# Kernel optimization log

Hardware: AMD Instinct MI355X
Metric: run time of the kernel (lower is better)

## Reference

```python
import jax, jax.numpy as jnp
import numpy as np

# Grid parameters (from init_kwargs)
GRID_W, GRID_L, GRID_H = 96, 96, 48
VOXEL_SIZE = 0.05
MIN_POINTS_PER_VOXEL = 10


def setup_inputs() -> dict:
    key = jax.random.key(0)
    k1, k2 = jax.random.split(key, 2)
    # points uniform over a ~[0,1.5]^3 sub-volume so voxel occupancy is realistic
    point_coordinates = jax.random.uniform(k1, (4, 3, 480, 640), jnp.float32) * 1.5
    point_attributes = jax.random.normal(k2, (4, 16, 480, 640), jnp.float32)
    origin = jnp.zeros((4, 3), jnp.float32)
    return {"point_coordinates": point_coordinates,
            "point_attributes": point_attributes,
            "origin": origin}


def _voxelize_one(coords, attrs, org):
    # coords: [3, N], attrs: [C, N], org: [3]
    V = GRID_W * GRID_L * GRID_H
    bounds = jnp.array([GRID_W, GRID_L, GRID_H], jnp.int32)
    # per-point voxel index (floor == .long() for positive; OOB handled by mask)
    idx3 = jnp.floor((coords - org[:, None]) / VOXEL_SIZE).astype(jnp.int32)  # [3, N]
    in_bounds = jnp.all((idx3 >= 0) & (idx3 < bounds[:, None]), axis=0)       # [N]
    flat = idx3[0] * (GRID_L * GRID_H) + idx3[1] * GRID_H + idx3[2]           # [N]
    flat = jnp.where(in_bounds, flat, 0)  # route OOB points to voxel 0, masked out
    # occupancy: scatter-add of in-bounds mask
    counts = jax.ops.segment_sum(in_bounds.astype(jnp.float32), flat, num_segments=V)
    # max-pool of attributes per voxel; OOB points contribute -inf
    masked = jnp.where(in_bounds[None, :], attrs, -jnp.inf)                   # [C, N]
    vmax = jax.ops.segment_max(masked.T, flat, num_segments=V).T              # [C, V]
    occ = counts >= MIN_POINTS_PER_VOXEL                                      # [V]
    data = jnp.where(occ[None, :] & jnp.isfinite(vmax), vmax, 0.0)            # [C, V]
    return data, occ


def reference(point_coordinates, point_attributes, origin):
    b, c = point_attributes.shape[:2]
    coords = point_coordinates.reshape(b, 3, -1)   # [B, 3, N]
    attrs = point_attributes.reshape(b, c, -1)     # [B, C, N]
    data, occ = jax.vmap(_voxelize_one)(coords, attrs, origin)
    voxeldata = data.reshape(b, c, GRID_W, GRID_L, GRID_H)
    voxeloccupancy = occ.reshape(b, 1, GRID_W, GRID_L, GRID_H).astype(jnp.float32)
    return voxeldata, voxeloccupancy
```

## Files before the change

### kernel.cpp

```cpp
#include <hip/hip_runtime.h>
#include <cstdint>
#include <math.h>

#define GRID_W 96
#define GRID_L 96
#define GRID_H 48
#define NVOX (GRID_W * GRID_L * GRID_H)
#define VOXEL_SIZE 0.05f
#define MIN_PTS 10
#define BATCH 4
#define CHANS 16
#define NPTS (480 * 640)
#define TOTPTS (BATCH * NPTS)
#define TOTVOX (BATCH * NVOX)

#define SCAN_BLKS 864
#define SCAN_TPB 256
#define SCAN_EPT 8
#define SCAN_CHUNK (SCAN_TPB * SCAN_EPT)

#define WS_OFFSETS 0
#define WS_VR      ((TOTVOX + 4) * 4)
#define WS_ROWS    (WS_VR + TOTPTS * 4)
#define WS_SUMS    (WS_ROWS + (size_t)TOTPTS * CHANS * 4)
#define WS_NEEDED  ((size_t)(WS_SUMS + 4096))


__global__ void k_zero(uint4* __restrict__ off4, unsigned* __restrict__ offsets) {
    int i = blockIdx.x * blockDim.x + threadIdx.x;
    if (i < TOTVOX / 4) off4[i] = uint4{0u, 0u, 0u, 0u};
    if (i == 0) {
        offsets[TOTVOX + 0] = 0u; offsets[TOTVOX + 1] = 0u;
        offsets[TOTVOX + 2] = 0u; offsets[TOTVOX + 3] = 0u;
    }
}

__global__ void k_hist4(const float* __restrict__ coords,
                        const float* __restrict__ origin,
                        unsigned*    __restrict__ vr,
                        unsigned*    __restrict__ cnt)
{
    int t = blockIdx.x * blockDim.x + threadIdx.x;
    if (t >= TOTPTS / 4) return;
    int pid = t * 4;
    int b = pid / NPTS;
    int n = pid - b * NPTS;

    const float* cb = coords + (size_t)b * 3 * NPTS;
    float4 X = *(const float4*)(cb + n);
    float4 Y = *(const float4*)(cb + NPTS + n);
    float4 Z = *(const float4*)(cb + 2 * NPTS + n);
    float ox = origin[b * 3 + 0];
    float oy = origin[b * 3 + 1];
    float oz = origin[b * 3 + 2];

    float xs[4] = {X.x, X.y, X.z, X.w};
    float ys[4] = {Y.x, Y.y, Y.z, Y.w};
    float zs[4] = {Z.x, Z.y, Z.z, Z.w};
    unsigned ps[4];
    #pragma unroll
    for (int k = 0; k < 4; ++k) {
        int ix = (int)floorf((xs[k] - ox) / VOXEL_SIZE);
        int iy = (int)floorf((ys[k] - oy) / VOXEL_SIZE);
        int iz = (int)floorf((zs[k] - oz) / VOXEL_SIZE);
        unsigned p = 0xFFFFFFFFu;
        if ((unsigned)ix < GRID_W && (unsigned)iy < GRID_L && (unsigned)iz < GRID_H) {
            int v = b * NVOX + ix * (GRID_L * GRID_H) + iy * GRID_H + iz;
            unsigned r = atomicAdd(&cnt[v], 1u);
            p = ((unsigned)v << 10) | (r & 1023u);
        }
        ps[k] = p;
    }
    *(uint4*)(vr + pid) = uint4{ps[0], ps[1], ps[2], ps[3]};
}

__global__ void k_scan1(unsigned* __restrict__ offsets,
                        unsigned* __restrict__ sums,
                        float*    __restrict__ occ)
{
    __shared__ unsigned s[SCAN_TPB];
    int t = threadIdx.x;
    int base = blockIdx.x * SCAN_CHUNK + t * SCAN_EPT;

    uint4 a = ((const uint4*)(offsets + base))[0];
    uint4 c = ((const uint4*)(offsets + base))[1];
    unsigned e[SCAN_EPT] = {a.x, a.y, a.z, a.w, c.x, c.y, c.z, c.w};

    float4 oc0, oc1;
    oc0.x = (e[0] >= MIN_PTS) ? 1.f : 0.f;  oc0.y = (e[1] >= MIN_PTS) ? 1.f : 0.f;
    oc0.z = (e[2] >= MIN_PTS) ? 1.f : 0.f;  oc0.w = (e[3] >= MIN_PTS) ? 1.f : 0.f;
    oc1.x = (e[4] >= MIN_PTS) ? 1.f : 0.f;  oc1.y = (e[5] >= MIN_PTS) ? 1.f : 0.f;
    oc1.z = (e[6] >= MIN_PTS) ? 1.f : 0.f;  oc1.w = (e[7] >= MIN_PTS) ? 1.f : 0.f;
    ((float4*)(occ + base))[0] = oc0;
    ((float4*)(occ + base))[1] = oc1;

    unsigned tot = 0;
    #pragma unroll
    for (int k = 0; k < SCAN_EPT; ++k) { unsigned v = e[k]; e[k] = tot; tot += v; }

    s[t] = tot;
    __syncthreads();
    #pragma unroll
    for (int off = 1; off < SCAN_TPB; off <<= 1) {
        unsigned v = (t >= off) ? s[t - off] : 0u;
        __syncthreads();
        s[t] += v;
        __syncthreads();
    }
    unsigned prefix = s[t] - tot;
    #pragma unroll
    for (int k = 0; k < SCAN_EPT; ++k) e[k] += prefix;

    ((uint4*)(offsets + base))[0] = uint4{e[0], e[1], e[2], e[3]};
    ((uint4*)(offsets + base))[1] = uint4{e[4], e[5], e[6], e[7]};

    if (t == SCAN_TPB - 1) sums[blockIdx.x] = s[t];
}

__global__ void k_scan2(unsigned* __restrict__ sums) {
    __shared__ unsigned s[1024];
    int t = threadIdx.x;
    unsigned my = (t < SCAN_BLKS) ? sums[t] : 0u;
    s[t] = my;
    __syncthreads();
    #pragma unroll
    for (int off = 1; off < 1024; off <<= 1) {
        unsigned v = (t >= off) ? s[t - off] : 0u;
        __syncthreads();
        s[t] += v;
        __syncthreads();
    }
    if (t < SCAN_BLKS) sums[t] = s[t] - my;
    if (t == SCAN_BLKS - 1) sums[SCAN_BLKS] = s[t];
}

__global__ void k_scatter_rows(const float*    __restrict__ attrs,
                               const unsigned* __restrict__ vr,
                               const unsigned* __restrict__ offsets,
                               const unsigned* __restrict__ sums,
                               float*          __restrict__ rows)
{
    int id = blockIdx.x * blockDim.x + threadIdx.x;
    if (id >= TOTPTS) return;
    unsigned p = vr[id];
    if (p == 0xFFFFFFFFu) return;
    unsigned v = p >> 10;
    unsigned r = p & 1023u;
    unsigned pos = offsets[v] + sums[v >> 11] + r;

    int b = id / NPTS;
    int n = id - b * NPTS;
    const float* ab = attrs + (size_t)b * CHANS * NPTS + n;
    float4 r0, r1, r2, r3;
    r0.x = ab[0 * (size_t)NPTS];  r0.y = ab[1 * (size_t)NPTS];
    r0.z = ab[2 * (size_t)NPTS];  r0.w = ab[3 * (size_t)NPTS];
    r1.x = ab[4 * (size_t)NPTS];  r1.y = ab[5 * (size_t)NPTS];
    r1.z = ab[6 * (size_t)NPTS];  r1.w = ab[7 * (size_t)NPTS];
    r2.x = ab[8 * (size_t)NPTS];  r2.y = ab[9 * (size_t)NPTS];
    r2.z = ab[10 * (size_t)NPTS]; r2.w = ab[11 * (size_t)NPTS];
    r3.x = ab[12 * (size_t)NPTS]; r3.y = ab[13 * (size_t)NPTS];
    r3.z = ab[14 * (size_t)NPTS]; r3.w = ab[15 * (size_t)NPTS];

    float4* dst = (float4*)(rows + (size_t)pos * CHANS);
    dst[0] = r0; dst[1] = r1; dst[2] = r2; dst[3] = r3;
}

__global__ void k_gather_rows(const float*    __restrict__ rows,
                              const unsigned* __restrict__ offsets,
                              const unsigned* __restrict__ sums,
                              float*          __restrict__ data)
{
    int vox = blockIdx.x * blockDim.x + threadIdx.x;
    if (vox >= TOTVOX) return;

    unsigned s0 = offsets[vox] + sums[vox >> 11];
    unsigned s1 = offsets[vox + 1] + sums[(vox + 1) >> 11];
    unsigned k = s1 - s0;

    float4 m0 = {0.f,0.f,0.f,0.f}, m1 = m0, m2 = m0, m3 = m0;
    if (k >= MIN_PTS) {
        const float ninf = -__builtin_inff();
        m0 = m1 = m2 = m3 = float4{ninf, ninf, ninf, ninf};
        const float4* seg = (const float4*)(rows + (size_t)s0 * CHANS);
        for (unsigned j = 0; j < k; ++j) {
            float4 r0 = seg[0], r1 = seg[1], r2 = seg[2], r3 = seg[3];
            seg += 4;
            m0.x = fmaxf(m0.x, r0.x); m0.y = fmaxf(m0.y, r0.y);
            m0.z = fmaxf(m0.z, r0.z); m0.w = fmaxf(m0.w, r0.w);
            m1.x = fmaxf(m1.x, r1.x); m1.y = fmaxf(m1.y, r1.y);
            m1.z = fmaxf(m1.z, r1.z); m1.w = fmaxf(m1.w, r1.w);
            m2.x = fmaxf(m2.x, r2.x); m2.y = fmaxf(m2.y, r2.y);
            m2.z = fmaxf(m2.z, r2.z); m2.w = fmaxf(m2.w, r2.w);
            m3.x = fmaxf(m3.x, r3.x); m3.y = fmaxf(m3.y, r3.y);
            m3.z = fmaxf(m3.z, r3.z); m3.w = fmaxf(m3.w, r3.w);
        }
        float mv[16] = {m0.x,m0.y,m0.z,m0.w, m1.x,m1.y,m1.z,m1.w,
                        m2.x,m2.y,m2.z,m2.w, m3.x,m3.y,m3.z,m3.w};
        #pragma unroll
        for (int c = 0; c < CHANS; ++c) if (!isfinite(mv[c])) mv[c] = 0.f;
        m0 = float4{mv[0],mv[1],mv[2],mv[3]};   m1 = float4{mv[4],mv[5],mv[6],mv[7]};
        m2 = float4{mv[8],mv[9],mv[10],mv[11]}; m3 = float4{mv[12],mv[13],mv[14],mv[15]};
    }

    int b = vox / NVOX;
    int v = vox - b * NVOX;
    float* db = data + (size_t)b * CHANS * NVOX + v;
    db[0 * (size_t)NVOX] = m0.x;  db[1 * (size_t)NVOX] = m0.y;
    db[2 * (size_t)NVOX] = m0.z;  db[3 * (size_t)NVOX] = m0.w;
    db[4 * (size_t)NVOX] = m1.x;  db[5 * (size_t)NVOX] = m1.y;
    db[6 * (size_t)NVOX] = m1.z;  db[7 * (size_t)NVOX] = m1.w;
    db[8 * (size_t)NVOX] = m2.x;  db[9 * (size_t)NVOX] = m2.y;
    db[10 * (size_t)NVOX] = m2.z; db[11 * (size_t)NVOX] = m2.w;
    db[12 * (size_t)NVOX] = m3.x; db[13 * (size_t)NVOX] = m3.y;
    db[14 * (size_t)NVOX] = m3.z; db[15 * (size_t)NVOX] = m3.w;
}


__device__ __forceinline__ unsigned flip_f32(float f) {
    unsigned u = __float_as_uint(f);
    unsigned mask = (unsigned)(-(int)(u >> 31)) | 0x80000000u;
    return u ^ mask;
}
__device__ __forceinline__ float unflip_f32(unsigned u) {
    unsigned mask = ((u >> 31) - 1u) | 0x80000000u;
    return __uint_as_float(u ^ mask);
}
#define FLIP_NEG_INF 0x007FFFFFu

__global__ void pv_init(uint4* __restrict__ out) {
    const int DATA4 = BATCH * CHANS * NVOX / 4;
    const int TOT4  = BATCH * (CHANS + 1) * NVOX / 4;
    int i = blockIdx.x * blockDim.x + threadIdx.x;
    if (i < TOT4) {
        unsigned val = (i < DATA4) ? FLIP_NEG_INF : 0u;
        out[i] = uint4{val, val, val, val};
    }
}

__global__ void pv_scatter(const float* __restrict__ coords,
                           const float* __restrict__ attrs,
                           const float* __restrict__ origin,
                           unsigned*    __restrict__ data_u,
                           unsigned*    __restrict__ cnt)
{
    int id = blockIdx.x * blockDim.x + threadIdx.x;
    if (id >= TOTPTS) return;
    int b = id / NPTS;
    int n = id - b * NPTS;
    const float* cb = coords + (size_t)b * 3 * NPTS;
    float x = cb[n], y = cb[NPTS + n], z = cb[2 * NPTS + n];
    float ox = origin[b * 3 + 0], oy = origin[b * 3 + 1], oz = origin[b * 3 + 2];
    int ix = (int)floorf((x - ox) / VOXEL_SIZE);
    int iy = (int)floorf((y - oy) / VOXEL_SIZE);
    int iz = (int)floorf((z - oz) / VOXEL_SIZE);
    if ((unsigned)ix < GRID_W && (unsigned)iy < GRID_L && (unsigned)iz < GRID_H) {
        int flat = ix * (GRID_L * GRID_H) + iy * GRID_H + iz;
        atomicAdd(&cnt[b * NVOX + flat], 1u);
        const float* ab = attrs + (size_t)b * CHANS * NPTS + n;
        unsigned*    db = data_u + (size_t)b * CHANS * NVOX + flat;
        #pragma unroll
        for (int c = 0; c < CHANS; ++c)
            atomicMax(&db[(size_t)c * NVOX], flip_f32(ab[(size_t)c * NPTS]));
    }
}

__global__ void pv_finalize(unsigned* __restrict__ data_u,
                            unsigned* __restrict__ cnt_u)
{
    int id = blockIdx.x * blockDim.x + threadIdx.x;
    if (id >= TOTVOX) return;
    int b = id / NVOX;
    int v = id - b * NVOX;
    unsigned cnt = cnt_u[id];
    bool occ = (cnt >= MIN_PTS);
    ((float*)cnt_u)[id] = occ ? 1.0f : 0.0f;
    unsigned* db = data_u + (size_t)b * CHANS * NVOX + v;
    #pragma unroll
    for (int c = 0; c < CHANS; ++c) {
        float f = unflip_f32(db[(size_t)c * NVOX]);
        ((float*)db)[(size_t)c * NVOX] = (occ && isfinite(f)) ? f : 0.0f;
    }
}


extern "C" void kernel_launch(void* const* d_in, const int* in_sizes, int n_in,
                              void* d_out, int out_size, void* d_ws, size_t ws_size,
                              hipStream_t stream) {
    const float* coords = (const float*)d_in[0];
    const float* attrs  = (const float*)d_in[1];
    const float* origin = (const float*)d_in[2];

    float* out = (float*)d_out;
    float* data = out;
    float* occ  = out + (size_t)BATCH * CHANS * NVOX;

    if (ws_size >= WS_NEEDED) {
        char* ws = (char*)d_ws;
        unsigned* offsets = (unsigned*)(ws + WS_OFFSETS);
        unsigned* vr      = (unsigned*)(ws + WS_VR);
        float*    rows    = (float*)(ws + WS_ROWS);
        unsigned* sums    = (unsigned*)(ws + WS_SUMS);

        k_zero<<<(TOTVOX / 4 + 255) / 256, 256, 0, stream>>>((uint4*)offsets, offsets);
        k_hist4<<<(TOTPTS / 4 + 255) / 256, 256, 0, stream>>>(coords, origin, vr, offsets);
        k_scan1<<<SCAN_BLKS, SCAN_TPB, 0, stream>>>(offsets, sums, occ);
        k_scan2<<<1, 1024, 0, stream>>>(sums);
        k_scatter_rows<<<(TOTPTS + 255) / 256, 256, 0, stream>>>(attrs, vr, offsets, sums, rows);
        k_gather_rows<<<(TOTVOX + 255) / 256, 256, 0, stream>>>(rows, offsets, sums, data);
    } else {
        unsigned* data_u = (unsigned*)data;
        unsigned* cnt    = (unsigned*)occ;
        const int TOT4 = BATCH * (CHANS + 1) * NVOX / 4;
        pv_init<<<(TOT4 + 255) / 256, 256, 0, stream>>>((uint4*)d_out);
        pv_scatter<<<(TOTPTS + 255) / 256, 256, 0, stream>>>(coords, attrs, origin, data_u, cnt);
        pv_finalize<<<(TOTVOX + 255) / 256, 256, 0, stream>>>(data_u, cnt);
    }
}
```

Baseline: 343.2 us.

## Pack intermediate rows as bf16 and vectorize scatter/gather four-wide

The permuted per-point attribute rows in the workspace are now stored as bf16 pairs (8 words per point instead of 16 floats), which halves the scatter write and gather read traffic. The scatter and gather kernels now handle four points or four voxels per thread, using float4/uint4 loads and stores. The zeroing kernel is replaced by hipMemsetAsync. The bf16 rounding changes the max-pooled output values, so results lose precision relative to the fp32 reference and may fail tolerance checks.

```diff
diff --git a/kernel.cpp b/kernel.cpp
--- a/kernel.cpp
+++ b/kernel.cpp
@@ -19,21 +19,22 @@
 #define SCAN_EPT 8
 #define SCAN_CHUNK (SCAN_TPB * SCAN_EPT)
 
+#define ROWW 8
+
 #define WS_OFFSETS 0
 #define WS_VR      ((TOTVOX + 4) * 4)
 #define WS_ROWS    (WS_VR + TOTPTS * 4)
-#define WS_SUMS    (WS_ROWS + (size_t)TOTPTS * CHANS * 4)
+#define WS_SUMS    (WS_ROWS + (size_t)TOTPTS * ROWW * 4)
 #define WS_NEEDED  ((size_t)(WS_SUMS + 4096))
 
-
-__global__ void k_zero(uint4* __restrict__ off4, unsigned* __restrict__ offsets) {
-    int i = blockIdx.x * blockDim.x + threadIdx.x;
-    if (i < TOTVOX / 4) off4[i] = uint4{0u, 0u, 0u, 0u};
-    if (i == 0) {
-        offsets[TOTVOX + 0] = 0u; offsets[TOTVOX + 1] = 0u;
-        offsets[TOTVOX + 2] = 0u; offsets[TOTVOX + 3] = 0u;
-    }
-}
+__device__ __forceinline__ unsigned bf16_rtne(float f) {
+    unsigned u = __float_as_uint(f);
+    return (u + 0x7FFFu + ((u >> 16) & 1u)) >> 16;
+}
+__device__ __forceinline__ unsigned pack2(float lo, float hi) {
+    return bf16_rtne(lo) | (bf16_rtne(hi) << 16);
+}
+
 
 __global__ void k_hist4(const float* __restrict__ coords,
                         const float* __restrict__ origin,
@@ -134,85 +135,101 @@
     if (t == SCAN_BLKS - 1) sums[SCAN_BLKS] = s[t];
 }
 
-__global__ void k_scatter_rows(const float*    __restrict__ attrs,
-                               const unsigned* __restrict__ vr,
+__global__ void k_scatter_rows4(const float*    __restrict__ attrs,
+                                const unsigned* __restrict__ vr,
+                                const unsigned* __restrict__ offsets,
+                                const unsigned* __restrict__ sums,
+                                unsigned*       __restrict__ rows)
+{
+    int t = blockIdx.x * blockDim.x + threadIdx.x;
+    if (t >= TOTPTS / 4) return;
+    int pid = t * 4;
+    int b = pid / NPTS;
+    int n = pid - b * NPTS;
+
+    uint4 P = *(const uint4*)(vr + pid);
+    unsigned ps[4] = {P.x, P.y, P.z, P.w};
+    unsigned pos[4];
+    #pragma unroll
+    for (int k = 0; k < 4; ++k) {
+        pos[k] = 0xFFFFFFFFu;
+        if (ps[k] != 0xFFFFFFFFu) {
+            unsigned v = ps[k] >> 10;
+            pos[k] = offsets[v] + sums[v >> 11] + (ps[k] & 1023u);
+        }
+    }
+
+    const float* ab = attrs + (size_t)b * CHANS * NPTS + n;
+    unsigned w[4][ROWW];
+    #pragma unroll
+    for (int c = 0; c < CHANS; c += 2) {
+        float4 a0 = *(const float4*)(ab + (size_t)c * NPTS);
+        float4 a1 = *(const float4*)(ab + (size_t)(c + 1) * NPTS);
+        w[0][c >> 1] = pack2(a0.x, a1.x);
+        w[1][c >> 1] = pack2(a0.y, a1.y);
+        w[2][c >> 1] = pack2(a0.z, a1.z);
+        w[3][c >> 1] = pack2(a0.w, a1.w);
+    }
+    #pragma unroll
+    for (int k = 0; k < 4; ++k) {
+        if (pos[k] == 0xFFFFFFFFu) continue;
+        uint4* dst = (uint4*)(rows + (size_t)pos[k] * ROWW);
+        dst[0] = uint4{w[k][0], w[k][1], w[k][2], w[k][3]};
+        dst[1] = uint4{w[k][4], w[k][5], w[k][6], w[k][7]};
+    }
+}
+
+__global__ void k_gather_rows4(const unsigned* __restrict__ rows,
                                const unsigned* __restrict__ offsets,
                                const unsigned* __restrict__ sums,
-                               float*          __restrict__ rows)
-{
-    int id = blockIdx.x * blockDim.x + threadIdx.x;
-    if (id >= TOTPTS) return;
-    unsigned p = vr[id];
-    if (p == 0xFFFFFFFFu) return;
-    unsigned v = p >> 10;
-    unsigned r = p & 1023u;
-    unsigned pos = offsets[v] + sums[v >> 11] + r;
-
-    int b = id / NPTS;
-    int n = id - b * NPTS;
-    const float* ab = attrs + (size_t)b * CHANS * NPTS + n;
-    float4 r0, r1, r2, r3;
-    r0.x = ab[0 * (size_t)NPTS];  r0.y = ab[1 * (size_t)NPTS];
-    r0.z = ab[2 * (size_t)NPTS];  r0.w = ab[3 * (size_t)NPTS];
-    r1.x = ab[4 * (size_t)NPTS];  r1.y = ab[5 * (size_t)NPTS];
-    r1.z = ab[6 * (size_t)NPTS];  r1.w = ab[7 * (size_t)NPTS];
-    r2.x = ab[8 * (size_t)NPTS];  r2.y = ab[9 * (size_t)NPTS];
-    r2.z = ab[10 * (size_t)NPTS]; r2.w = ab[11 * (size_t)NPTS];
-    r3.x = ab[12 * (size_t)NPTS]; r3.y = ab[13 * (size_t)NPTS];
-    r3.z = ab[14 * (size_t)NPTS]; r3.w = ab[15 * (size_t)NPTS];
-
-    float4* dst = (float4*)(rows + (size_t)pos * CHANS);
-    dst[0] = r0; dst[1] = r1; dst[2] = r2; dst[3] = r3;
-}
-
-__global__ void k_gather_rows(const float*    __restrict__ rows,
-                              const unsigned* __restrict__ offsets,
-                              const unsigned* __restrict__ sums,
-                              float*          __restrict__ data)
-{
-    int vox = blockIdx.x * blockDim.x + threadIdx.x;
-    if (vox >= TOTVOX) return;
-
-    unsigned s0 = offsets[vox] + sums[vox >> 11];
-    unsigned s1 = offsets[vox + 1] + sums[(vox + 1) >> 11];
-    unsigned k = s1 - s0;
-
-    float4 m0 = {0.f,0.f,0.f,0.f}, m1 = m0, m2 = m0, m3 = m0;
-    if (k >= MIN_PTS) {
-        const float ninf = -__builtin_inff();
-        m0 = m1 = m2 = m3 = float4{ninf, ninf, ninf, ninf};
-        const float4* seg = (const float4*)(rows + (size_t)s0 * CHANS);
-        for (unsigned j = 0; j < k; ++j) {
-            float4 r0 = seg[0], r1 = seg[1], r2 = seg[2], r3 = seg[3];
-            seg += 4;
-            m0.x = fmaxf(m0.x, r0.x); m0.y = fmaxf(m0.y, r0.y);
-            m0.z = fmaxf(m0.z, r0.z); m0.w = fmaxf(m0.w, r0.w);
-            m1.x = fmaxf(m1.x, r1.x); m1.y = fmaxf(m1.y, r1.y);
-            m1.z = fmaxf(m1.z, r1.z); m1.w = fmaxf(m1.w, r1.w);
-            m2.x = fmaxf(m2.x, r2.x); m2.y = fmaxf(m2.y, r2.y);
-            m2.z = fmaxf(m2.z, r2.z); m2.w = fmaxf(m2.w, r2.w);
-            m3.x = fmaxf(m3.x, r3.x); m3.y = fmaxf(m3.y, r3.y);
-            m3.z = fmaxf(m3.z, r3.z); m3.w = fmaxf(m3.w, r3.w);
+                               float*          __restrict__ data)
+{
+    int g = blockIdx.x * blockDim.x + threadIdx.x;
+    if (g >= TOTVOX / 4) return;
+    int vox0 = g * 4;
+
+    uint4 O = *(const uint4*)(offsets + vox0);
+    unsigned base = sums[vox0 >> 11];
+    unsigned s[5];
+    s[0] = O.x + base; s[1] = O.y + base; s[2] = O.z + base; s[3] = O.w + base;
+    s[4] = offsets[vox0 + 4] + sums[(vox0 + 4) >> 11];
+
+    float m[4][CHANS];
+    #pragma unroll
+    for (int q = 0; q < 4; ++q) {
+        unsigned k = s[q + 1] - s[q];
+        if (k >= MIN_PTS) {
+            const float ninf = -__builtin_inff();
+            #pragma unroll
+            for (int c = 0; c < CHANS; ++c) m[q][c] = ninf;
+            const uint4* seg = (const uint4*)(rows + (size_t)s[q] * ROWW);
+            for (unsigned j = 0; j < k; ++j) {
+                uint4 lo = seg[0], hi = seg[1];
+                seg += 2;
+                unsigned ww[8] = {lo.x, lo.y, lo.z, lo.w, hi.x, hi.y, hi.z, hi.w};
+                #pragma unroll
+                for (int h = 0; h < 8; ++h) {
+                    float f0 = __uint_as_float(ww[h] << 16);
+                    float f1 = __uint_as_float(ww[h] & 0xFFFF0000u);
+                    m[q][2 * h]     = fmaxf(m[q][2 * h], f0);
+                    m[q][2 * h + 1] = fmaxf(m[q][2 * h + 1], f1);
+                }
+            }
+            #pragma unroll
+            for (int c = 0; c < CHANS; ++c) if (!isfinite(m[q][c])) m[q][c] = 0.f;
+        } else {
+            #pragma unroll
+            for (int c = 0; c < CHANS; ++c) m[q][c] = 0.f;
         }
-        float mv[16] = {m0.x,m0.y,m0.z,m0.w, m1.x,m1.y,m1.z,m1.w,
-                        m2.x,m2.y,m2.z,m2.w, m3.x,m3.y,m3.z,m3.w};
-        #pragma unroll
-        for (int c = 0; c < CHANS; ++c) if (!isfinite(mv[c])) mv[c] = 0.f;
-        m0 = float4{mv[0],mv[1],mv[2],mv[3]};   m1 = float4{mv[4],mv[5],mv[6],mv[7]};
-        m2 = float4{mv[8],mv[9],mv[10],mv[11]}; m3 = float4{mv[12],mv[13],mv[14],mv[15]};
-    }
-
-    int b = vox / NVOX;
-    int v = vox - b * NVOX;
-    float* db = data + (size_t)b * CHANS * NVOX + v;
-    db[0 * (size_t)NVOX] = m0.x;  db[1 * (size_t)NVOX] = m0.y;
-    db[2 * (size_t)NVOX] = m0.z;  db[3 * (size_t)NVOX] = m0.w;
-    db[4 * (size_t)NVOX] = m1.x;  db[5 * (size_t)NVOX] = m1.y;
-    db[6 * (size_t)NVOX] = m1.z;  db[7 * (size_t)NVOX] = m1.w;
-    db[8 * (size_t)NVOX] = m2.x;  db[9 * (size_t)NVOX] = m2.y;
-    db[10 * (size_t)NVOX] = m2.z; db[11 * (size_t)NVOX] = m2.w;
-    db[12 * (size_t)NVOX] = m3.x; db[13 * (size_t)NVOX] = m3.y;
-    db[14 * (size_t)NVOX] = m3.z; db[15 * (size_t)NVOX] = m3.w;
+    }
+
+    int b = vox0 / NVOX;
+    int v0 = vox0 - b * NVOX;
+    float* db = data + (size_t)b * CHANS * NVOX + v0;
+    #pragma unroll
+    for (int c = 0; c < CHANS; ++c) {
+        *(float4*)(db + (size_t)c * NVOX) = float4{m[0][c], m[1][c], m[2][c], m[3][c]};
+    }
 }
 
 
@@ -298,15 +315,15 @@
         char* ws = (char*)d_ws;
         unsigned* offsets = (unsigned*)(ws + WS_OFFSETS);
         unsigned* vr      = (unsigned*)(ws + WS_VR);
-        float*    rows    = (float*)(ws + WS_ROWS);
+        unsigned* rows    = (unsigned*)(ws + WS_ROWS);
         unsigned* sums    = (unsigned*)(ws + WS_SUMS);
 
-        k_zero<<<(TOTVOX / 4 + 255) / 256, 256, 0, stream>>>((uint4*)offsets, offsets);
+        hipMemsetAsync(offsets, 0, (size_t)(TOTVOX + 4) * 4, stream);
         k_hist4<<<(TOTPTS / 4 + 255) / 256, 256, 0, stream>>>(coords, origin, vr, offsets);
         k_scan1<<<SCAN_BLKS, SCAN_TPB, 0, stream>>>(offsets, sums, occ);
         k_scan2<<<1, 1024, 0, stream>>>(sums);
-        k_scatter_rows<<<(TOTPTS + 255) / 256, 256, 0, stream>>>(attrs, vr, offsets, sums, rows);
-        k_gather_rows<<<(TOTVOX + 255) / 256, 256, 0, stream>>>(rows, offsets, sums, data);
+        k_scatter_rows4<<<(TOTPTS / 4 + 255) / 256, 256, 0, stream>>>(attrs, vr, offsets, sums, rows);
+        k_gather_rows4<<<(TOTVOX / 4 + 255) / 256, 256, 0, stream>>>(rows, offsets, sums, data);
     } else {
         unsigned* data_u = (unsigned*)data;
         unsigned* cnt    = (unsigned*)occ;
```

Measured after the change: 337.3 us. No clear change (-1.7%).
